# Kernel optimization log

Hardware: AMD Instinct MI355X
Metric: run time of the kernel (lower is better)

Reference implementation:

```python
import jax, jax.numpy as jnp
import numpy as np

N_BINS = 15  # matches __init__ default


def setup_inputs() -> dict:
    key = jax.random.key(0)
    k1, k2 = jax.random.split(key)
    N, C = 100000, 1000
    softmaxes_probs = jax.random.uniform(k1, (N, C), dtype=jnp.float32)
    labels = jax.random.randint(k2, (N,), 0, C, dtype=jnp.int64)
    return {"softmaxes_probs": softmaxes_probs, "labels": labels}


def reference(softmaxes_probs, labels):
    # Classwise ECE: for each class c and bin b = (b/n_bins, (b+1)/n_bins],
    #   sce_c = sum_b |avg_conf_in_bin - acc_in_bin| * (count_in_bin / N)
    # returned value is mean_c sce_c.
    n_bins = N_BINS
    N, C = softmaxes_probs.shape
    conf = softmaxes_probs  # [N, C]

    # bin index: conf in (b/n_bins, (b+1)/n_bins] -> b ; conf <= 0 -> -1 (no bin)
    bin_idx = jnp.ceil(conf * n_bins).astype(jnp.int32) - 1
    bin_idx = jnp.minimum(bin_idx, n_bins - 1)
    valid = bin_idx >= 0

    class_ids = jnp.arange(C, dtype=jnp.int32)[None, :]  # [1, C]
    # combined segment id per (sample, class); invalid entries go to a dump segment
    seg = jnp.where(valid, bin_idx + class_ids * n_bins, C * n_bins)  # [N, C]
    seg_flat = seg.ravel()
    num_seg = C * n_bins + 1

    ones = jnp.ones_like(conf)
    counts = jax.ops.segment_sum(ones.ravel(), seg_flat, num_segments=num_seg)[:-1].reshape(C, n_bins)
    conf_sum = jax.ops.segment_sum(conf.ravel(), seg_flat, num_segments=num_seg)[:-1].reshape(C, n_bins)
    # labels_in_class broadcast to [N, C]
    correct = (labels[:, None] == jnp.arange(C, dtype=labels.dtype)[None, :]).astype(conf.dtype)
    correct_sum = jax.ops.segment_sum(correct.ravel(), seg_flat, num_segments=num_seg)[:-1].reshape(C, n_bins)

    prop_in_bin = counts / N  # prop_in_bin = in_bin.float().mean() over N samples
    nonempty = counts > 0
    denom = jnp.maximum(counts, 1.0)
    acc_in_bin = correct_sum / denom
    avg_conf_in_bin = conf_sum / denom
    contrib = jnp.where(nonempty, jnp.abs(avg_conf_in_bin - acc_in_bin) * prop_in_bin, 0.0)
    per_class_sce = jnp.sum(contrib, axis=1)  # [C]
    return jnp.mean(per_class_sce)
```

## Files before the change

### kernel.cpp

```cpp
#include <hip/hip_runtime.h>


#define NBINS   15
#define THREADS 512
#define PSTRIDE 31
#define LDSW    (THREADS * PSTRIDE)
#define SLAB    (1024 * NBINS)
#define SLABH   (SLAB / 2)
#define RBLK    120
#define Q40     1099511627776.0f

__global__ __launch_bounds__(THREADS, 4) void ece_hist(
    const float* __restrict__ probs, const int* __restrict__ labels,
    int N, int C, int R,
    unsigned* __restrict__ partial,
    unsigned long long* __restrict__ accum,
    unsigned* __restrict__ doneCnt)
{
    __shared__ unsigned sA[LDSW];
    const int t = threadIdx.x;
    if (blockIdx.x == 0 && t == 0) { *accum = 0ull; *doneCnt = 0u; }
    #pragma unroll
    for (int i = t; i < LDSW; i += THREADS) sA[i] = 0u;
    __syncthreads();

    const int cls0 = 2 * t;
    const bool live = (cls0 + 1 < C);
    const int col  = live ? cls0 : 0;

    const int r0 = blockIdx.x * R;
    int rend = N - r0; if (rend > R) rend = R; if (rend < 0) rend = 0;

    const float2* p = (const float2*)(probs + (size_t)r0 * C + col);
    const size_t rowstep = (size_t)(C >> 1);
    unsigned* s0 = sA + t * PSTRIDE;

    float2 bufA[8], bufB[8];
    int    labA[8], labB[8];

    #define LOADG(buf, lab, base)                                          \
        _Pragma("unroll")                                                  \
        for (int k = 0; k < 8; ++k) {                                      \
            int ri = (base) + k;                                           \
            ri = ri < rend ? ri : rend - 1;                                \
            buf[k] = live ? p[(size_t)ri * rowstep] : make_float2(0.f,0.f);\
            lab[k] = labels[r0 + ri];                                      \
        }

    #define PROC1(v, lb)                                                   \
        {                                                                  \
            int b0 = (int)(v.x * 15.0f);   \
            b0 = b0 < NBINS - 1 ? b0 : NBINS - 1;                          \
            unsigned c0 = (unsigned)fmaf(v.x, 128.0f, 0.5f);               \
            c0 += ((lb) == cls0) ? (unsigned)(-128) : 0u;                  \
            atomicAdd(&s0[b0], (v.x > 0.0f) ? c0 : 0u);                    \
            int b1 = (int)(v.y * 15.0f);                                   \
            b1 = b1 < NBINS - 1 ? b1 : NBINS - 1;                          \
            unsigned c1 = (unsigned)fmaf(v.y, 128.0f, 0.5f);               \
            c1 += ((lb) == cls0 + 1) ? (unsigned)(-128) : 0u;              \
            atomicAdd(&s0[NBINS + b1], (v.y > 0.0f) ? c1 : 0u);            \
        }

    #define PROCG(buf, lab)                                                \
        _Pragma("unroll")                                                  \
        for (int k = 0; k < 8; ++k) PROC1(buf[k], lab[k])

    int r = 0;
    if (rend >= 16) {
        LOADG(bufA, labA, 0);
        for (; r + 16 <= rend; r += 16) {
            LOADG(bufB, labB, r + 8);
            PROCG(bufA, labA);
            LOADG(bufA, labA, r + 16);
            PROCG(bufB, labB);
        }
    }
    for (; r < rend; ++r) {
        float2 v = live ? p[(size_t)r * rowstep] : make_float2(0.f, 0.f);
        int lb = labels[r0 + r];
        PROC1(v, lb);
    }
    __syncthreads();

    unsigned* dst = partial + (size_t)blockIdx.x * SLABH;
    #pragma unroll
    for (int i = t; i < SLABH; i += THREADS) {
        int owner = i / 15, j = 2 * (i - owner * 15);
        unsigned v0 = sA[owner * PSTRIDE + j];
        unsigned v1 = sA[owner * PSTRIDE + j + 1];
        dst[i] = (v0 & 0xFFFFu) | (v1 << 16);
    }
}

__global__ __launch_bounds__(1024, 1) void ece_red(
    const unsigned* __restrict__ partial, int chunks, int C, int N,
    unsigned long long* __restrict__ accum, unsigned* __restrict__ doneCnt,
    float* __restrict__ out)
{
    __shared__ int sq0[16][64];
    __shared__ int sq1[16][64];
    const int t = threadIdx.x;
    const int g = t >> 6, pj = t & 63;
    const int pair = blockIdx.x * 64 + pj;

    const int gsz = (chunks + 15) >> 4;
    int k0 = g * gsz;
    int k1 = k0 + gsz; if (k1 > chunks) k1 = chunks;
    int a0 = 0, a1 = 0;
    #pragma unroll 8
    for (int k = k0; k < k1; ++k) {
        unsigned w = partial[(size_t)k * SLABH + pair];
        a0 += (int)(short)(w & 0xFFFFu);
        a1 += (int)(short)(w >> 16);
    }
    sq0[g][pj] = a0;
    sq1[g][pj] = a1;
    __syncthreads();

    if (t < 64) {
        int t0 = 0, t1 = 0;
        #pragma unroll
        for (int gg = 0; gg < 16; ++gg) { t0 += sq0[gg][t]; t1 += sq1[gg][t]; }
        int slot0 = (blockIdx.x * 64 + t) * 2;
        float contrib = 0.0f;
        if (slot0     < C * NBINS) contrib += fabsf((float)t0);
        if (slot0 + 1 < C * NBINS) contrib += fabsf((float)t1);
        contrib *= (1.0f / 128.0f) * (1.0f / (float)N);
        for (int o = 32; o; o >>= 1) contrib += __shfl_down(contrib, o);
        if (t == 0) {
            atomicAdd(accum, (unsigned long long)(contrib * Q40));
            __threadfence();
            if (atomicAdd(doneCnt, 1u) == (unsigned)(RBLK - 1)) {
                __threadfence();
                unsigned long long a = atomicAdd(accum, 0ull);
                out[0] = (float)((double)a * (1.0 / (double)Q40) / (double)C);
            }
        }
    }
}

extern "C" void kernel_launch(void* const* d_in, const int* in_sizes, int n_in,
                              void* d_out, int out_size, void* d_ws, size_t ws_size,
                              hipStream_t stream) {
    const float* probs  = (const float*)d_in[0];
    const int*   labels = (const int*)d_in[1];
    const int N = in_sizes[1];
    const int C = in_sizes[0] / N;

    const size_t headBytes = 4096;
    const size_t slabBytes = (size_t)SLABH * 4;

    unsigned long long* accum   = (unsigned long long*)d_ws;
    unsigned*           doneCnt = (unsigned*)((char*)d_ws + 8);
    unsigned*           partial = (unsigned*)((char*)d_ws + headBytes);

    long long avail = (long long)ws_size - (long long)headBytes;
    int chunks = (int)(avail / (long long)slabBytes);
    if (chunks > 512) chunks = 512;
    if (chunks < 393) chunks = 393;
    const int R = (N + chunks - 1) / chunks;

    ece_hist<<<chunks, THREADS, 0, stream>>>(probs, labels, N, C, R,
                                             partial, accum, doneCnt);
    ece_red<<<RBLK, 1024, 0, stream>>>(partial, chunks, C, N,
                                       accum, doneCnt, (float*)d_out);
}
```

Before: 89.14 us.

## Pack two classes per LDS word and track correct counts in byte bins

Each thread's per-class histogram now packs both classes into the low and high 16-bit halves of one LDS word. This roughly halves the per-thread LDS footprint (stride 31 to 17), and launch bounds rise from 4 to 6 blocks per SM. The -128 correction for correct labels moves to a separate shared array of byte counters, updated only when the label matches, and is subtracted when the partial slab is written out. The goal is higher occupancy and fewer LDS atomics per element. The risks are that 8-bit correct counters could overflow for large row chunks and that 16-bit halves could carry into each other before the fix-up.

```diff
diff --git a/kernel.cpp b/kernel.cpp
--- a/kernel.cpp
+++ b/kernel.cpp
@@ -3,14 +3,14 @@
 
 #define NBINS   15
 #define THREADS 512
-#define PSTRIDE 31
+#define PSTRIDE 17
 #define LDSW    (THREADS * PSTRIDE)
-#define SLAB    (1024 * NBINS)
-#define SLABH   (SLAB / 2)
+#define CORW    3840
+#define SLABH   (THREADS * NBINS)
 #define RBLK    120
 #define Q40     1099511627776.0f
 
-__global__ __launch_bounds__(THREADS, 4) void ece_hist(
+__global__ __launch_bounds__(THREADS, 6) void ece_hist(
     const float* __restrict__ probs, const int* __restrict__ labels,
     int N, int C, int R,
     unsigned* __restrict__ partial,
@@ -18,10 +18,13 @@
     unsigned* __restrict__ doneCnt)
 {
     __shared__ unsigned sA[LDSW];
+    __shared__ unsigned sCorW[CORW];
     const int t = threadIdx.x;
     if (blockIdx.x == 0 && t == 0) { *accum = 0ull; *doneCnt = 0u; }
     #pragma unroll
     for (int i = t; i < LDSW; i += THREADS) sA[i] = 0u;
+    #pragma unroll
+    for (int i = t; i < CORW; i += THREADS) sCorW[i] = 0u;
     __syncthreads();
 
     const int cls0 = 2 * t;
@@ -52,13 +55,18 @@
             int b0 = (int)(v.x * 15.0f);   \
             b0 = b0 < NBINS - 1 ? b0 : NBINS - 1;                          \
             unsigned c0 = (unsigned)fmaf(v.x, 128.0f, 0.5f);               \
-            c0 += ((lb) == cls0) ? (unsigned)(-128) : 0u;                  \
             atomicAdd(&s0[b0], (v.x > 0.0f) ? c0 : 0u);                    \
             int b1 = (int)(v.y * 15.0f);                                   \
             b1 = b1 < NBINS - 1 ? b1 : NBINS - 1;                          \
             unsigned c1 = (unsigned)fmaf(v.y, 128.0f, 0.5f);               \
-            c1 += ((lb) == cls0 + 1) ? (unsigned)(-128) : 0u;              \
-            atomicAdd(&s0[NBINS + b1], (v.y > 0.0f) ? c1 : 0u);            \
+            atomicAdd(&s0[b1], (v.y > 0.0f) ? (c1 << 16) : 0u);            \
+            if ((lb) == cls0 && v.x > 0.0f) {                              \
+                int sl = (lb) * NBINS + b0;                                \
+                atomicAdd(&sCorW[sl >> 2], 1u << (8 * (sl & 3)));          \
+            } else if ((lb) == cls0 + 1 && v.y > 0.0f) {                   \
+                int sl = (lb) * NBINS + b1;                                \
+                atomicAdd(&sCorW[sl >> 2], 1u << (8 * (sl & 3)));          \
+            }                                                              \
         }
 
     #define PROCG(buf, lab)                                                \
@@ -82,13 +90,15 @@
     }
     __syncthreads();
 
+    const unsigned char* sCorB = (const unsigned char*)sCorW;
     unsigned* dst = partial + (size_t)blockIdx.x * SLABH;
     #pragma unroll
     for (int i = t; i < SLABH; i += THREADS) {
-        int owner = i / 15, j = 2 * (i - owner * 15);
-        unsigned v0 = sA[owner * PSTRIDE + j];
-        unsigned v1 = sA[owner * PSTRIDE + j + 1];
-        dst[i] = (v0 & 0xFFFFu) | (v1 << 16);
+        int o = i / NBINS, j = i - o * NBINS;
+        unsigned w = sA[o * PSTRIDE + j];
+        int s0c = (int)(w & 0xFFFFu) - 128 * (int)sCorB[(2 * o) * NBINS + j];
+        int s1c = (int)(w >> 16)     - 128 * (int)sCorB[(2 * o + 1) * NBINS + j];
+        dst[i] = ((unsigned)s0c & 0xFFFFu) | ((unsigned)s1c << 16);
     }
 }
 
@@ -121,12 +131,13 @@
         int t0 = 0, t1 = 0;
         #pragma unroll
         for (int gg = 0; gg < 16; ++gg) { t0 += sq0[gg][t]; t1 += sq1[gg][t]; }
-        int slot0 = (blockIdx.x * 64 + t) * 2;
+        int pr = blockIdx.x * 64 + t;
+        int o  = pr / NBINS;
         float contrib = 0.0f;
-        if (slot0     < C * NBINS) contrib += fabsf((float)t0);
-        if (slot0 + 1 < C * NBINS) contrib += fabsf((float)t1);
+        if (2 * o     < C) contrib += fabsf((float)t0);
+        if (2 * o + 1 < C) contrib += fabsf((float)t1);
         contrib *= (1.0f / 128.0f) * (1.0f / (float)N);
-        for (int o = 32; o; o >>= 1) contrib += __shfl_down(contrib, o);
+        for (int off = 32; off; off >>= 1) contrib += __shfl_down(contrib, off);
         if (t == 0) {
             atomicAdd(accum, (unsigned long long)(contrib * Q40));
             __threadfence();
```

Measured after the change: 94.33 us. +5.8%, slower.
